# Kernel optimization log

Measured on AMD Instinct MI355X. Metric: run time of the kernel, lower is better.

Reference implementation:

```python
import jax, jax.numpy as jnp
import numpy as np
import math

IMG = 256      # image H = W (img_shape)
N_ANG = 360    # projection views over [0, pi)
N_DET = 256    # radial detector bins
N_SAMP = 256   # samples along each ray
VOX = 2.0      # voxel size / detector bin width in mm (isotropic)
FWHM = 4.0     # gaussian_PSF FWHM in mm


def _gauss_kernel(sigma):
    radius = max(1, int(math.ceil(3.0 * sigma)))
    t = np.arange(-radius, radius + 1, dtype=np.float64)
    k = np.exp(-0.5 * (t / sigma) ** 2)
    return (k / k.sum()).astype(np.float32), radius


def _blur_axis(x, sigma, axis):
    """1-D Gaussian blur with reflect padding along `axis` (static small kernel)."""
    k, r = _gauss_kernel(sigma)
    x = jnp.moveaxis(x, axis, -1)
    L = x.shape[-1]
    pad = [(0, 0)] * (x.ndim - 1) + [(r, r)]
    xp = jnp.pad(x, pad, mode='reflect')
    out = sum(float(k[i]) * xp[..., i:i + L] for i in range(2 * r + 1))
    return jnp.moveaxis(out, -1, axis)


def _blur2d(x, sigma):
    return _blur_axis(_blur_axis(x, sigma, -1), sigma, -2)


def _geometry():
    """Static parallel-beam ray-sampling geometry (bilinear taps, in pixel units)."""
    theta = np.pi * np.arange(N_ANG) / N_ANG
    r = (np.arange(N_DET) - (N_DET - 1) / 2.0) * VOX   # detector offsets [mm]
    s = (np.arange(N_SAMP) - (N_SAMP - 1) / 2.0) * VOX  # depth along ray [mm]
    cos = np.cos(theta)[:, None, None]
    sin = np.sin(theta)[:, None, None]
    x = r[None, :, None] * cos - s[None, None, :] * sin  # (A, D, S) mm
    y = r[None, :, None] * sin + s[None, None, :] * cos
    ix = x / VOX + (IMG - 1) / 2.0
    iy = y / VOX + (IMG - 1) / 2.0
    valid = ((ix >= 0) & (ix <= IMG - 1) & (iy >= 0) & (iy <= IMG - 1)).astype(np.float32)
    j0 = np.clip(np.floor(ix).astype(np.int32), 0, IMG - 2)
    i0 = np.clip(np.floor(iy).astype(np.int32), 0, IMG - 2)
    fx = (ix - j0).astype(np.float32)
    fy = (iy - i0).astype(np.float32)
    return i0, j0, fy, fx, valid

_GEO = tuple(jnp.asarray(a) for a in _geometry())


def _project(img):
    """Parallel-view 2D ray projection: img (B,H,W) -> sinogram (B, N_DET, N_ANG)."""
    i0, j0, fy, fx, valid = _GEO
    v00 = img[:, i0, j0]
    v01 = img[:, i0, j0 + 1]
    v10 = img[:, i0 + 1, j0]
    v11 = img[:, i0 + 1, j0 + 1]
    vals = ((1 - fy) * (1 - fx) * v00 + (1 - fy) * fx * v01
            + fy * (1 - fx) * v10 + fy * fx * v11) * valid
    sino = vals.sum(-1) * VOX          # (B, N_ANG, N_DET), line integral in mm
    return jnp.transpose(sino, (0, 2, 1))  # (B, N_DET, N_ANG)


def setup_inputs() -> dict:
    key = jax.random.key(0)
    k1, k2 = jax.random.split(key)
    image = jax.random.uniform(k1, (2, 1, IMG, IMG), dtype=jnp.float32)
    attenuation_map = jax.random.uniform(k2, (2, 1, IMG, IMG), dtype=jnp.float32)
    return {"image": image, "attenuation_map": attenuation_map}


def reference(image, attenuation_map):
    sqrt_log2 = math.sqrt(math.log(2.0))
    sigma_img = (FWHM / (4.0 * sqrt_log2)) / VOX
    # emission PSF blur (reflect) then project
    img_b = _blur2d(image, sigma_img)
    sino = _project(img_b[:, 0])[:, None]          # (B,1,N_DET,N_ANG)
    # attenuation: wider PSF blur, 0.01 scale, project, exponential scaling
    sigma_att = (FWHM / (2.0 * sqrt_log2)) / VOX
    att_b = _blur2d(attenuation_map, sigma_att) * 0.01
    att_sino = _project(att_b[:, 0])[:, None]
    sino = sino * jnp.exp(-att_sino * VOX)
    # column-wise (detector axis) sinogram PSF
    sino = _blur_axis(sino, sigma_img, -2)
    return sino
```

## Files before the change

kernel.cpp:

```cpp
#include <hip/hip_runtime.h>
#include <math.h>

#define IMG 256
#define N_ANG 360
#define N_DET 256

#define NH_BLOCKS 181
#define NV_BLOCKS (179 * 32)
#define EPS 1e-3f

struct W9 { float w[9]; };
struct AngTab { double c, sn; float cf, snf; float pad0, pad1; };

typedef _Float16 h2 __attribute__((ext_vector_type(2)));

#if __has_builtin(__builtin_amdgcn_fdot2)
__device__ __forceinline__ float fdot2(h2 a, h2 b, float c) {
    return __builtin_amdgcn_fdot2(a, b, c, false);
}
#else
__device__ __forceinline__ float fdot2(h2 a, h2 b, float c) {
    return c + (float)a[0] * (float)b[0] + (float)a[1] * (float)b[1];
}
#endif

__device__ __forceinline__ h2 as_h2(unsigned u) { return __builtin_bit_cast(h2, u); }
__device__ __forceinline__ unsigned pack2(float a, float b) {
    h2 v = { (_Float16)a, (_Float16)b };
    return __builtin_bit_cast(unsigned, v);
}

__device__ __forceinline__ int refl(int i, int L) {
    if (i < 0) i = -i;
    if (i >= L) i = 2 * (L - 1) - i;
    return i;
}

__global__ void blur4_k(const float* __restrict__ img, const float* __restrict__ att,
                        float* __restrict__ pk, W9 wi, W9 wa) {
    int x = threadIdx.x, y = blockIdx.x, m = blockIdx.y;
    const float* src = ((m & 1) ? att : img) + (m >> 1) * IMG * IMG;
    const float* w = (m & 1) ? wa.w : wi.w;
    float scale = (m & 1) ? 0.01f : 1.0f;
    float acc = 0.f;
    for (int dy = -4; dy <= 4; ++dy) {
        float wy = w[dy + 4];
        if (wy == 0.f) continue;
        const float* rowp = src + refl(y + dy, IMG) * IMG;
        float ra = 0.f;
        for (int dx = -4; dx <= 4; ++dx) ra += w[dx + 4] * rowp[refl(x + dx, IMG)];
        acc += wy * ra;
    }
    pk[(y * IMG + x) * 4 + m] = acc * scale;
}

__global__ void quad_k(const float4* __restrict__ pk, uint4* __restrict__ quad,
                       AngTab* __restrict__ tab) {
    int j = threadIdx.x, i = blockIdx.x;
    int gid = i * IMG + j;
    if (gid < N_ANG) {
        double th = M_PI * (double)gid / 360.0;
        double c = cos(th), sn = sin(th);
        AngTab tb;
        tb.c = c; tb.sn = sn; tb.cf = (float)c; tb.snf = (float)sn;
        tb.pad0 = 0.f; tb.pad1 = 0.f;
        tab[gid] = tb;
    }
    int jn = min(j + 1, IMG - 1), in_ = min(i + 1, IMG - 1);
    float4 p00 = pk[i * IMG + j],   p01 = pk[i * IMG + jn];
    float4 p10 = pk[in_ * IMG + j], p11 = pk[in_ * IMG + jn];
    uint4 qa, qb;
    qa.x = pack2(p00.x, p01.x); qa.y = pack2(p10.x, p11.x);
    qa.z = pack2(p00.y, p01.y); qa.w = pack2(p10.y, p11.y);
    qb.x = pack2(p00.z, p01.z); qb.y = pack2(p10.z, p11.z);
    qb.z = pack2(p00.w, p01.w); qb.w = pack2(p10.w, p11.w);
    int p = i * IMG + j;
    quad[2 * p] = qa;
    quad[2 * p + 1] = qb;
}

template <typename P>
__device__ __forceinline__ int lastTrue(P p) {
    if (!p(0)) return -1;
    if (p(255)) return 255;
    int lo = 0, hi = 255;
    while (lo < hi) { int m = (lo + hi + 1) >> 1; if (p(m)) lo = m; else hi = m - 1; }
    return lo;
}
template <typename P>
__device__ __forceinline__ int firstTrue(P p) {
    if (!p(255)) return 256;
    if (p(0)) return 0;
    int lo = 0, hi = 255;
    while (lo < hi) { int m = (lo + hi) >> 1; if (p(m)) hi = m; else lo = m + 1; }
    return lo;
}

__device__ __forceinline__ void tap_acc(const uint4* __restrict__ quad,
                                        int i0, int j0,
                                        float w00, float w01, float w10, float w11,
                                        float4& acc) {
    h2 wt = { (_Float16)w00, (_Float16)w01 };
    h2 wb = { (_Float16)w10, (_Float16)w11 };
    const uint4* q = quad + 2 * ((i0 << 8) + j0);
    uint4 qa = q[0], qb = q[1];
    acc.x = fdot2(as_h2(qa.x), wt, acc.x);
    acc.x = fdot2(as_h2(qa.y), wb, acc.x);
    acc.y = fdot2(as_h2(qa.z), wt, acc.y);
    acc.y = fdot2(as_h2(qa.w), wb, acc.y);
    acc.z = fdot2(as_h2(qb.x), wt, acc.z);
    acc.z = fdot2(as_h2(qb.y), wb, acc.z);
    acc.w = fdot2(as_h2(qb.z), wt, acc.w);
    acc.w = fdot2(as_h2(qb.w), wb, acc.w);
}

__global__ __launch_bounds__(512) void proj_k(const uint4* __restrict__ quad,
                                              const AngTab* __restrict__ tab,
                                              float4* __restrict__ part4,
                                              float* __restrict__ out, W9 wblur) {
    int t = threadIdx.x;
    int bx = blockIdx.x;

    if (bx < NH_BLOCKS) {
        int d = t & 255, kc = t >> 8;
        int a = (bx <= 90) ? bx : bx + 179;
        AngTab tb = tab[a];
        double rr = (double)(2 * d - 255);
        double rc = __dmul_rn(rr, tb.c), rs = __dmul_rn(rr, tb.sn);

        auto evIx = [&](int k) -> double {
            double ss = (double)(2 * k - 255);
            return __dadd_rn(__dmul_rn(__dsub_rn(rc, __dmul_rn(ss, tb.sn)), 0.5), 127.5);
        };
        auto evIy = [&](int k) -> double {
            double ss = (double)(2 * k - 255);
            return __dadd_rn(__dmul_rn(__dadd_rn(rs, __dmul_rn(ss, tb.c)), 0.5), 127.5);
        };
        int khiA = lastTrue([&](int k) { return evIx(k) >= 0.0; });
        int kloA = firstTrue([&](int k) { return evIx(k) <= 255.0; });
        int kloB, khiB;
        if (tb.c > 0.0) {
            kloB = firstTrue([&](int k) { return evIy(k) >= 0.0; });
            khiB = lastTrue([&](int k) { return evIy(k) <= 255.0; });
        } else {
            khiB = lastTrue([&](int k) { return evIy(k) >= 0.0; });
            kloB = firstTrue([&](int k) { return evIy(k) <= 255.0; });
        }
        int lo = max(kloA, kloB), hi = min(khiA, khiB);
        lo = max(lo, kc * 128); hi = min(hi, kc * 128 + 127);
        if (lo > hi) { lo = 0; hi = -1; }

        int jl = (hi >= lo) ? lo : 0x7fffffff;
        int jh = (hi >= lo) ? hi : (-0x7fffffff - 1);
        #pragma unroll
        for (int off = 32; off; off >>= 1) {
            jl = min(jl, __shfl_xor(jl, off));
            jh = max(jh, __shfl_xor(jh, off));
        }

        float x0f = (float)evIx(128);
        float y0f = (float)evIy(128);
        float dxf = -tb.snf, dyf = tb.cf;

        float4 acc = make_float4(0.f, 0.f, 0.f, 0.f);
        for (int kb = jl; kb <= jh; kb += 4) {
            #pragma unroll
            for (int u = 0; u < 4; ++u) {
                int k = kb + u;
                float kf = (float)(k - 128);
                float ixf = fmaf(kf, dxf, x0f);
                float iyf = fmaf(kf, dyf, y0f);
                float m = (k >= lo && k <= hi) ? 2.0f : 0.0f;
                int j0 = (int)ixf; j0 = min(max(j0, 0), 254);
                int i0 = (int)iyf; i0 = min(max(i0, 0), 254);
                float fx = ixf - (float)j0;
                float fy = iyf - (float)i0;
                float gxm = (1.f - fx) * m, fxm = fx * m;
                float gy = 1.f - fy;
                tap_acc(quad, i0, j0, gy * gxm, gy * fxm, fy * gxm, fy * fxm, acc);
            }
        }

        __shared__ float4 red[512];
        __shared__ float vb[2][N_DET];
        red[t] = acc;
        __syncthreads();
        if (t < 256) {
            float4 u = red[t], v = red[t + 256];
            float si0 = u.x + v.x, sa0 = u.y + v.y;
            float si1 = u.z + v.z, sa1 = u.w + v.w;
            vb[0][t] = si0 * expf(-sa0 * 2.0f);
            vb[1][t] = si1 * expf(-sa1 * 2.0f);
        }
        __syncthreads();
        if (t < 256) {
            float a0 = 0.f, a1 = 0.f;
            #pragma unroll
            for (int i = -2; i <= 2; ++i) {
                int dd = refl(t + i, N_DET);
                a0 += wblur.w[i + 2] * vb[0][dd];
                a1 += wblur.w[i + 2] * vb[1][dd];
            }
            out[t * N_ANG + a] = a0;
            out[(N_DET + t) * N_ANG + a] = a1;
        }
    } else {
        int idx = bx - NH_BLOCKS;
        int a = 91 + (idx >> 5);
        int dgrp = idx & 31;
        int lane = t & 63, w = t >> 6;
        int d = dgrp * 8 + w;
        AngTab tb = tab[a];
        float cf = tb.cf, snf = tb.snf;
        float df = (float)d - 127.5f;
        float hx = fmaf(df, cf, 127.5f);
        float hy = fmaf(df, snf, 127.5f);

        float4 acc = make_float4(0.f, 0.f, 0.f, 0.f);
        #pragma unroll
        for (int j = 0; j < 4; ++j) {
            int k = j * 64 + lane;
            float kf = (float)k - 127.5f;
            float ixf = fmaf(-kf, snf, hx);
            float iyf = fmaf(kf, cf, hy);
            float vmin = fminf(fminf(ixf, 255.0f - ixf), fminf(iyf, 255.0f - iyf));
            if (!__any(vmin > -EPS)) continue;
            float m = (vmin >= EPS) ? 2.0f : 0.0f;
            if (fabsf(vmin) < EPS) {
                double ss = (double)(2 * k - 255);
                double rr = (double)(2 * d - 255);
                double rc = __dmul_rn(rr, tb.c), rs = __dmul_rn(rr, tb.sn);
                double ixd = __dadd_rn(__dmul_rn(__dsub_rn(rc, __dmul_rn(ss, tb.sn)), 0.5), 127.5);
                double iyd = __dadd_rn(__dmul_rn(__dadd_rn(rs, __dmul_rn(ss, tb.c)), 0.5), 127.5);
                bool v = (ixd >= 0.0) && (ixd <= 255.0) && (iyd >= 0.0) && (iyd <= 255.0);
                m = v ? 2.0f : 0.0f;
            }
            int j0 = (int)ixf; j0 = min(max(j0, 0), 254);
            int i0 = (int)iyf; i0 = min(max(i0, 0), 254);
            float fx = ixf - (float)j0;
            float fy = iyf - (float)i0;
            float gxm = (1.f - fx) * m, fxm = fx * m;
            float gy = 1.f - fy;
            tap_acc(quad, i0, j0, gy * gxm, gy * fxm, fy * gxm, fy * fxm, acc);
        }

        #pragma unroll
        for (int off = 32; off; off >>= 1) {
            acc.x += __shfl_xor(acc.x, off);
            acc.y += __shfl_xor(acc.y, off);
            acc.z += __shfl_xor(acc.z, off);
            acc.w += __shfl_xor(acc.w, off);
        }
        if (lane == 0) part4[a * N_DET + d] = acc;
    }
}

__global__ __launch_bounds__(256) void finish_v_k(const float4* __restrict__ part4,
                                                  float* __restrict__ out, W9 wt) {
    int d = threadIdx.x;
    int b = blockIdx.x / 179;
    int a = 91 + (blockIdx.x % 179);
    float4 s = part4[a * N_DET + d];
    float si = b ? s.z : s.x;
    float sa = b ? s.w : s.y;
    __shared__ float vb[N_DET];
    vb[d] = si * expf(-sa * 2.0f);
    __syncthreads();
    float acc = 0.f;
    #pragma unroll
    for (int i = -2; i <= 2; ++i) acc += wt.w[i + 2] * vb[refl(d + i, N_DET)];
    out[(b * N_DET + d) * N_ANG + a] = acc;
}

static void gauss_w(W9* wt, double sigma, int r, int pad_to_center4) {
    double tmp[9];
    double s = 0.0;
    for (int i = -r; i <= r; ++i) {
        double v = exp(-0.5 * ((double)i / sigma) * ((double)i / sigma));
        tmp[i + r] = v;
        s += v;
    }
    for (int i = 0; i < 9; ++i) wt->w[i] = 0.f;
    int off = pad_to_center4 ? (4 - r) : 0;
    for (int i = 0; i < 2 * r + 1; ++i) wt->w[i + off] = (float)(tmp[i] / s);
}

extern "C" void kernel_launch(void* const* d_in, const int* in_sizes, int n_in,
                              void* d_out, int out_size, void* d_ws, size_t ws_size,
                              hipStream_t stream) {
    const float* img = (const float*)d_in[0];
    const float* att = (const float*)d_in[1];
    float* out = (float*)d_out;

    char* ws = (char*)d_ws;
    AngTab* tab = (AngTab*)ws;
    float* pk = (float*)(ws + 16384);
    uint4* quad = (uint4*)(ws + 16384 + (1 << 20));
    float4* part4 = (float4*)(ws + 16384 + 3 * (1 << 20));

    double sqrt_log2 = sqrt(log(2.0));
    double sigma_img = 4.0 / (4.0 * sqrt_log2) / 2.0;
    double sigma_att = 4.0 / (2.0 * sqrt_log2) / 2.0;
    W9 wimg_pad, wimg, watt;
    gauss_w(&wimg_pad, sigma_img, 2, 1);
    gauss_w(&wimg, sigma_img, 2, 0);
    gauss_w(&watt, sigma_att, 4, 0);

    blur4_k<<<dim3(IMG, 4), IMG, 0, stream>>>(img, att, pk, wimg_pad, watt);
    quad_k<<<IMG, IMG, 0, stream>>>((const float4*)pk, quad, tab);
    proj_k<<<NH_BLOCKS + NV_BLOCKS, 512, 0, stream>>>(quad, tab, part4, out, wimg);
    finish_v_k<<<2 * 179, N_DET, 0, stream>>>(part4, out, wimg);
}
```

Baseline: 61.95 us.

## Split horizontal-ray projection blocks across depth tiles with atomic accumulation

```diff
diff --git a/kernel.cpp b/kernel.cpp
--- a/kernel.cpp
+++ b/kernel.cpp
@@ -5,7 +5,8 @@
 #define N_ANG 360
 #define N_DET 256
 
-#define NH_BLOCKS 181
+#define KT 4
+#define NH_BLOCKS (181 * KT)
 #define NV_BLOCKS (179 * 32)
 #define EPS 1e-3f
 
@@ -54,8 +55,27 @@
     pk[(y * IMG + x) * 4 + m] = acc * scale;
 }
 
-__global__ void quad_k(const float4* __restrict__ pk, uint4* __restrict__ quad,
-                       AngTab* __restrict__ tab) {
+template <typename P>
+__device__ __forceinline__ int lastTrue(P p) {
+    if (!p(0)) return -1;
+    if (p(255)) return 255;
+    int lo = 0, hi = 255;
+    while (lo < hi) { int m = (lo + hi + 1) >> 1; if (p(m)) lo = m; else hi = m - 1; }
+    return lo;
+}
+template <typename P>
+__device__ __forceinline__ int firstTrue(P p) {
+    if (!p(255)) return 256;
+    if (p(0)) return 0;
+    int lo = 0, hi = 255;
+    while (lo < hi) { int m = (lo + hi) >> 1; if (p(m)) hi = m; else lo = m + 1; }
+    return lo;
+}
+
+__global__ void quad_k(const float4* __restrict__ pk,
+                       uint4* __restrict__ quadI, uint4* __restrict__ quadA,
+                       AngTab* __restrict__ tab,
+                       int2* __restrict__ ivl, float2* __restrict__ pos0) {
     int j = threadIdx.x, i = blockIdx.x;
     int gid = i * IMG + j;
     if (gid < N_ANG) {
@@ -69,85 +89,83 @@
     int jn = min(j + 1, IMG - 1), in_ = min(i + 1, IMG - 1);
     float4 p00 = pk[i * IMG + j],   p01 = pk[i * IMG + jn];
     float4 p10 = pk[in_ * IMG + j], p11 = pk[in_ * IMG + jn];
-    uint4 qa, qb;
-    qa.x = pack2(p00.x, p01.x); qa.y = pack2(p10.x, p11.x);
-    qa.z = pack2(p00.y, p01.y); qa.w = pack2(p10.y, p11.y);
-    qb.x = pack2(p00.z, p01.z); qb.y = pack2(p10.z, p11.z);
-    qb.z = pack2(p00.w, p01.w); qb.w = pack2(p10.w, p11.w);
-    int p = i * IMG + j;
-    quad[2 * p] = qa;
-    quad[2 * p + 1] = qb;
-}
-
-template <typename P>
-__device__ __forceinline__ int lastTrue(P p) {
-    if (!p(0)) return -1;
-    if (p(255)) return 255;
-    int lo = 0, hi = 255;
-    while (lo < hi) { int m = (lo + hi + 1) >> 1; if (p(m)) lo = m; else hi = m - 1; }
-    return lo;
-}
-template <typename P>
-__device__ __forceinline__ int firstTrue(P p) {
-    if (!p(255)) return 256;
-    if (p(0)) return 0;
-    int lo = 0, hi = 255;
-    while (lo < hi) { int m = (lo + hi) >> 1; if (p(m)) hi = m; else lo = m + 1; }
-    return lo;
-}
-
-__device__ __forceinline__ void tap_acc(const uint4* __restrict__ quad,
-                                        int i0, int j0,
-                                        float w00, float w01, float w10, float w11,
-                                        float4& acc) {
-    h2 wt = { (_Float16)w00, (_Float16)w01 };
-    h2 wb = { (_Float16)w10, (_Float16)w11 };
-    const uint4* q = quad + 2 * ((i0 << 8) + j0);
-    uint4 qa = q[0], qb = q[1];
-    acc.x = fdot2(as_h2(qa.x), wt, acc.x);
-    acc.x = fdot2(as_h2(qa.y), wb, acc.x);
-    acc.y = fdot2(as_h2(qa.z), wt, acc.y);
-    acc.y = fdot2(as_h2(qa.w), wb, acc.y);
-    acc.z = fdot2(as_h2(qb.x), wt, acc.z);
-    acc.z = fdot2(as_h2(qb.y), wb, acc.z);
-    acc.w = fdot2(as_h2(qb.z), wt, acc.w);
-    acc.w = fdot2(as_h2(qb.w), wb, acc.w);
-}
-
-__global__ __launch_bounds__(512) void proj_k(const uint4* __restrict__ quad,
-                                              const AngTab* __restrict__ tab,
-                                              float4* __restrict__ part4,
-                                              float* __restrict__ out, W9 wblur) {
-    int t = threadIdx.x;
-    int bx = blockIdx.x;
-
-    if (bx < NH_BLOCKS) {
-        int d = t & 255, kc = t >> 8;
-        int a = (bx <= 90) ? bx : bx + 179;
-        AngTab tb = tab[a];
+    uint4 qi, qa;
+    qi.x = pack2(p00.x, p01.x); qi.y = pack2(p10.x, p11.x);
+    qi.z = pack2(p00.z, p01.z); qi.w = pack2(p10.z, p11.z);
+    qa.x = pack2(p00.y, p01.y); qa.y = pack2(p10.y, p11.y);
+    qa.z = pack2(p00.w, p01.w); qa.w = pack2(p10.w, p11.w);
+    quadI[gid] = qi;
+    quadA[gid] = qa;
+
+    if (i < 181) {
+        int aidx = i, d = j;
+        int a = (aidx <= 90) ? aidx : aidx + 179;
+        double th = M_PI * (double)a / 360.0;
+        double c = cos(th), sn = sin(th);
         double rr = (double)(2 * d - 255);
-        double rc = __dmul_rn(rr, tb.c), rs = __dmul_rn(rr, tb.sn);
-
+        double rc = __dmul_rn(rr, c), rs = __dmul_rn(rr, sn);
         auto evIx = [&](int k) -> double {
             double ss = (double)(2 * k - 255);
-            return __dadd_rn(__dmul_rn(__dsub_rn(rc, __dmul_rn(ss, tb.sn)), 0.5), 127.5);
+            return __dadd_rn(__dmul_rn(__dsub_rn(rc, __dmul_rn(ss, sn)), 0.5), 127.5);
         };
         auto evIy = [&](int k) -> double {
             double ss = (double)(2 * k - 255);
-            return __dadd_rn(__dmul_rn(__dadd_rn(rs, __dmul_rn(ss, tb.c)), 0.5), 127.5);
+            return __dadd_rn(__dmul_rn(__dadd_rn(rs, __dmul_rn(ss, c)), 0.5), 127.5);
         };
         int khiA = lastTrue([&](int k) { return evIx(k) >= 0.0; });
         int kloA = firstTrue([&](int k) { return evIx(k) <= 255.0; });
         int kloB, khiB;
-        if (tb.c > 0.0) {
+        if (c > 0.0) {
             kloB = firstTrue([&](int k) { return evIy(k) >= 0.0; });
             khiB = lastTrue([&](int k) { return evIy(k) <= 255.0; });
         } else {
             khiB = lastTrue([&](int k) { return evIy(k) >= 0.0; });
             kloB = firstTrue([&](int k) { return evIy(k) <= 255.0; });
         }
-        int lo = max(kloA, kloB), hi = min(khiA, khiB);
-        lo = max(lo, kc * 128); hi = min(hi, kc * 128 + 127);
+        int ray = aidx * N_DET + d;
+        ivl[ray] = make_int2(max(kloA, kloB), min(khiA, khiB));
+        pos0[ray] = make_float2((float)evIx(128), (float)evIy(128));
+    }
+}
+
+__device__ __forceinline__ void tap_acc(const uint4* __restrict__ quadI,
+                                        const uint4* __restrict__ quadA,
+                                        int off,
+                                        float w00, float w01, float w10, float w11,
+                                        float4& acc) {
+    h2 wt = { (_Float16)w00, (_Float16)w01 };
+    h2 wb = { (_Float16)w10, (_Float16)w11 };
+    uint4 qi = quadI[off], qa = quadA[off];
+    acc.x = fdot2(as_h2(qi.x), wt, acc.x);
+    acc.x = fdot2(as_h2(qi.y), wb, acc.x);
+    acc.z = fdot2(as_h2(qi.z), wt, acc.z);
+    acc.z = fdot2(as_h2(qi.w), wb, acc.z);
+    acc.y = fdot2(as_h2(qa.x), wt, acc.y);
+    acc.y = fdot2(as_h2(qa.y), wb, acc.y);
+    acc.w = fdot2(as_h2(qa.z), wt, acc.w);
+    acc.w = fdot2(as_h2(qa.w), wb, acc.w);
+}
+
+__global__ __launch_bounds__(512) void proj_k(const uint4* __restrict__ quadI,
+                                              const uint4* __restrict__ quadA,
+                                              const AngTab* __restrict__ tab,
+                                              const int2* __restrict__ ivl,
+                                              const float2* __restrict__ pos0,
+                                              float* __restrict__ part4) {
+    int t = threadIdx.x;
+    int bx = blockIdx.x;
+
+    if (bx < NH_BLOCKS) {
+        int d = t & 255, kc = t >> 8;
+        int aidx = bx % 181, kt = bx / 181;
+        int a = (aidx <= 90) ? aidx : aidx + 179;
+        AngTab tb = tab[a];
+        int ray = aidx * N_DET + d;
+        int2 iv = ivl[ray];
+        float2 p0 = pos0[ray];
+
+        int base = (kt * 2 + kc) * 32;
+        int lo = max(iv.x, base), hi = min(iv.y, base + 31);
         if (lo > hi) { lo = 0; hi = -1; }
 
         int jl = (hi >= lo) ? lo : 0x7fffffff;
@@ -158,8 +176,6 @@
             jh = max(jh, __shfl_xor(jh, off));
         }
 
-        float x0f = (float)evIx(128);
-        float y0f = (float)evIy(128);
         float dxf = -tb.snf, dyf = tb.cf;
 
         float4 acc = make_float4(0.f, 0.f, 0.f, 0.f);
@@ -168,8 +184,8 @@
             for (int u = 0; u < 4; ++u) {
                 int k = kb + u;
                 float kf = (float)(k - 128);
-                float ixf = fmaf(kf, dxf, x0f);
-                float iyf = fmaf(kf, dyf, y0f);
+                float ixf = fmaf(kf, dxf, p0.x);
+                float iyf = fmaf(kf, dyf, p0.y);
                 float m = (k >= lo && k <= hi) ? 2.0f : 0.0f;
                 int j0 = (int)ixf; j0 = min(max(j0, 0), 254);
                 int i0 = (int)iyf; i0 = min(max(i0, 0), 254);
@@ -177,32 +193,21 @@
                 float fy = iyf - (float)i0;
                 float gxm = (1.f - fx) * m, fxm = fx * m;
                 float gy = 1.f - fy;
-                tap_acc(quad, i0, j0, gy * gxm, gy * fxm, fy * gxm, fy * fxm, acc);
+                tap_acc(quadI, quadA, (i0 << 8) + j0,
+                        gy * gxm, gy * fxm, fy * gxm, fy * fxm, acc);
             }
         }
 
         __shared__ float4 red[512];
-        __shared__ float vb[2][N_DET];
         red[t] = acc;
         __syncthreads();
         if (t < 256) {
             float4 u = red[t], v = red[t + 256];
-            float si0 = u.x + v.x, sa0 = u.y + v.y;
-            float si1 = u.z + v.z, sa1 = u.w + v.w;
-            vb[0][t] = si0 * expf(-sa0 * 2.0f);
-            vb[1][t] = si1 * expf(-sa1 * 2.0f);
-        }
-        __syncthreads();
-        if (t < 256) {
-            float a0 = 0.f, a1 = 0.f;
-            #pragma unroll
-            for (int i = -2; i <= 2; ++i) {
-                int dd = refl(t + i, N_DET);
-                a0 += wblur.w[i + 2] * vb[0][dd];
-                a1 += wblur.w[i + 2] * vb[1][dd];
-            }
-            out[t * N_ANG + a] = a0;
-            out[(N_DET + t) * N_ANG + a] = a1;
+            float* dst = part4 + (a * N_DET + t) * 4;
+            atomicAdd(dst + 0, u.x + v.x);
+            atomicAdd(dst + 1, u.y + v.y);
+            atomicAdd(dst + 2, u.z + v.z);
+            atomicAdd(dst + 3, u.w + v.w);
         }
     } else {
         int idx = bx - NH_BLOCKS;
@@ -241,7 +246,8 @@
             float fy = iyf - (float)i0;
             float gxm = (1.f - fx) * m, fxm = fx * m;
             float gy = 1.f - fy;
-            tap_acc(quad, i0, j0, gy * gxm, gy * fxm, fy * gxm, fy * fxm, acc);
+            tap_acc(quadI, quadA, (i0 << 8) + j0,
+                    gy * gxm, gy * fxm, fy * gxm, fy * fxm, acc);
         }
 
         #pragma unroll
@@ -251,15 +257,15 @@
             acc.z += __shfl_xor(acc.z, off);
             acc.w += __shfl_xor(acc.w, off);
         }
-        if (lane == 0) part4[a * N_DET + d] = acc;
-    }
-}
-
-__global__ __launch_bounds__(256) void finish_v_k(const float4* __restrict__ part4,
-                                                  float* __restrict__ out, W9 wt) {
+        if (lane == 0) ((float4*)part4)[a * N_DET + d] = acc;
+    }
+}
+
+__global__ __launch_bounds__(256) void finish_k(const float4* __restrict__ part4,
+                                                float* __restrict__ out, W9 wt) {
     int d = threadIdx.x;
-    int b = blockIdx.x / 179;
-    int a = 91 + (blockIdx.x % 179);
+    int b = blockIdx.x / N_ANG;
+    int a = blockIdx.x % N_ANG;
     float4 s = part4[a * N_DET + d];
     float si = b ? s.z : s.x;
     float sa = b ? s.w : s.y;
@@ -293,10 +299,13 @@
     float* out = (float*)d_out;
 
     char* ws = (char*)d_ws;
-    AngTab* tab = (AngTab*)ws;
-    float* pk = (float*)(ws + 16384);
-    uint4* quad = (uint4*)(ws + 16384 + (1 << 20));
-    float4* part4 = (float4*)(ws + 16384 + 3 * (1 << 20));
+    AngTab* tab   = (AngTab*)ws;
+    uint4* quadI  = (uint4*)(ws + 16384);
+    uint4* quadA  = (uint4*)(ws + 16384 + (1 << 20));
+    int2* ivl     = (int2*)(ws + 16384 + 2 * (1 << 20));
+    float2* pos0  = (float2*)(ws + 16384 + 2 * (1 << 20) + (1 << 19));
+    float* pk     = (float*)(ws + 16384 + 3 * (1 << 20));
+    float* part4  = (float*)(ws + 16384 + 4 * (1 << 20));
 
     double sqrt_log2 = sqrt(log(2.0));
     double sigma_img = 4.0 / (4.0 * sqrt_log2) / 2.0;
@@ -306,8 +315,9 @@
     gauss_w(&wimg, sigma_img, 2, 0);
     gauss_w(&watt, sigma_att, 4, 0);
 
+    hipMemsetAsync(part4, 0, N_ANG * N_DET * 4 * sizeof(float), stream);
     blur4_k<<<dim3(IMG, 4), IMG, 0, stream>>>(img, att, pk, wimg_pad, watt);
-    quad_k<<<IMG, IMG, 0, stream>>>((const float4*)pk, quad, tab);
-    proj_k<<<NH_BLOCKS + NV_BLOCKS, 512, 0, stream>>>(quad, tab, part4, out, wimg);
-    finish_v_k<<<2 * 179, N_DET, 0, stream>>>(part4, out, wimg);
-}
+    quad_k<<<IMG, IMG, 0, stream>>>((const float4*)pk, quadI, quadA, tab, ivl, pos0);
+    proj_k<<<NH_BLOCKS + NV_BLOCKS, 512, 0, stream>>>(quadI, quadA, tab, ivl, pos0, part4);
+    finish_k<<<2 * N_ANG, N_DET, 0, stream>>>((const float4*)part4, out, wimg);
+}
```

Measured after the change: 79.14 us. 27.7% more time.
